# Performance work log

Hardware: AMD Instinct MI355X
Metric: run time of the kernel (lower is better)

The kernel has to match this reference:

```python
import jax, jax.numpy as jnp
import numpy as np

DIM = 256
NUM_HEADS = 4
HEAD_DIM = DIM // NUM_HEADS


def setup_inputs() -> dict:
    key = jax.random.key(0)
    ks = jax.random.split(key, 8)
    B, N, C = 4, 2048, DIM
    x = jax.random.normal(ks[0], (B, N, C), dtype=jnp.float32)
    R = jax.random.normal(ks[1], (B, 3, 3), dtype=jnp.float32)
    P = jax.random.normal(ks[2], (N, 3), dtype=jnp.float32)
    s = 1.0 / np.sqrt(C)
    qkv_w = jax.random.normal(ks[3], (3 * C, C), dtype=jnp.float32) * s
    qkv_b = jax.random.normal(ks[4], (3 * C,), dtype=jnp.float32) * 0.02
    proj_w = jax.random.normal(ks[5], (C, C), dtype=jnp.float32) * s
    proj_b = jax.random.normal(ks[6], (C,), dtype=jnp.float32) * 0.02
    pos_scale = jnp.asarray(1.0, dtype=jnp.float32)
    return {"x": x, "R": R, "P": P, "qkv_w": qkv_w, "qkv_b": qkv_b,
            "proj_w": proj_w, "proj_b": proj_b, "pos_scale": pos_scale}


def reference(x, R, P, qkv_w, qkv_b, proj_w, proj_b, pos_scale):
    B, N, C = x.shape
    H, D = NUM_HEADS, HEAD_DIM
    scale = D ** -0.5
    # qkv: (B,N,3C) -> (3,B,H,N,D)
    qkv = (x @ qkv_w.T + qkv_b).reshape(B, N, 3, H, D).transpose(2, 0, 3, 1, 4)
    q, k, v = qkv[0], qkv[1], qkv[2]
    # attention logits (B,H,N,N)
    attn = jnp.einsum('bhid,bhjd->bhij', q, k) * scale
    # positional bias: RP = (R @ P^T)^T -> (B,N,3); bias_ij = dot(RP_i, P_j)
    RP = jnp.einsum('bab,jb->bja', R, P) if False else jnp.einsum('bca,ja->bjc', jnp.swapaxes(R, 1, 2), P)
    RP = jnp.einsum('bcd,jd->bjc', R, P)  # (B,N,3): (R @ P.T).T
    bias = jnp.einsum('bik,jk->bij', RP, P)[:, None, :, :] * pos_scale  # (B,1,N,N) broadcast over heads
    attn = jax.nn.softmax(attn + bias, axis=-1)
    out = jnp.einsum('bhij,bhjd->bhid', attn, v)  # (B,H,N,D)
    out = out.transpose(0, 2, 1, 3).reshape(B, N, C)
    out = out @ proj_w.T + proj_b
    return out
```

## Files before the change

kernel.cpp:

```cpp
#include <hip/hip_runtime.h>
#include <hip/hip_bf16.h>

#define B_ 4
#define N_ 2048
#define C_ 256
#define H_ 4
#define D_ 64

typedef __attribute__((ext_vector_type(8))) short bf16x8;
typedef __attribute__((ext_vector_type(4))) float f32x4;

#define LOG2E 1.4426950408889634f

static __device__ inline unsigned short f2bf(float f) {
    unsigned u = __builtin_bit_cast(unsigned, f);
    unsigned r = (u + 0x7fffu + ((u >> 16) & 1u)) >> 16;
    return (unsigned short)r;
}
static __device__ inline float bf2f(unsigned short h) {
    unsigned u = ((unsigned)h) << 16;
    return __builtin_bit_cast(float, u);
}
static __device__ inline unsigned pack2(float a, float b) {
    __hip_bfloat162 h = __float22bfloat162_rn(make_float2(a, b));
    unsigned u;
    __builtin_memcpy(&u, &h, 4);
    return u;
}
static __device__ inline bf16x8 ld_frag(const unsigned short* p) {
    return __builtin_bit_cast(bf16x8, *(const uint4*)p);
}

__global__ __launch_bounds__(256) void prep_kernel(
    const float* __restrict__ x, const float* __restrict__ qkv_w,
    const float* __restrict__ proj_w, const float* __restrict__ Pm,
    unsigned short* __restrict__ xb, unsigned short* __restrict__ wqb,
    unsigned short* __restrict__ wpb, unsigned short* __restrict__ Pext)
{
    const int bid = blockIdx.x, tid = threadIdx.x;
    const float* s; unsigned short* d; int i;
    if (bid < 1024)      { s = x;      d = xb;  i = (bid * 256 + tid) * 8; }
    else if (bid < 1120) { s = qkv_w;  d = wqb; i = ((bid - 1024) * 256 + tid) * 8; }
    else if (bid < 1152) { s = proj_w; d = wpb; i = ((bid - 1120) * 256 + tid) * 8; }
    else {
        int n = (bid - 1152) * 256 + tid;
        if (n >= N_) return;
        unsigned short row[32];
        #pragma unroll
        for (int q = 0; q < 32; ++q) row[q] = 0;
        #pragma unroll
        for (int c = 0; c < 3; ++c) {
            float p = Pm[n * 3 + c];
            unsigned short u = f2bf(p);
            unsigned short v = f2bf(p - bf2f(u));
            row[c] = u; row[3 + c] = v; row[6 + c] = u;
        }
        #pragma unroll
        for (int q = 0; q < 4; ++q)
            *(uint4*)&Pext[(size_t)n * 32 + q * 8] = *(const uint4*)&row[q * 8];
        return;
    }
    float4 a = *(const float4*)(s + i);
    float4 b = *(const float4*)(s + i + 4);
    uint4 u;
    u.x = pack2(a.x, a.y); u.y = pack2(a.z, a.w);
    u.z = pack2(b.x, b.y); u.w = pack2(b.z, b.w);
    *(uint4*)(d + i) = u;
}

__global__ __launch_bounds__(256) void qkv_gemm(
    const unsigned short* __restrict__ xb, const unsigned short* __restrict__ wb,
    const float* __restrict__ bias, unsigned short* __restrict__ qb,
    unsigned short* __restrict__ kb, unsigned short* __restrict__ vt)
{
    __shared__ __align__(16) unsigned short As[128 * 40];
    __shared__ __align__(16) unsigned short Bs[64 * 40];
    const int m0 = blockIdx.x * 128, o0 = blockIdx.y * 64;
    const int tid = threadIdx.x;
    const int wave = tid >> 6, lane = tid & 63, quad = lane >> 4, l16 = lane & 15;

    f32x4 acc[2][4];
    #pragma unroll
    for (int i = 0; i < 2; ++i)
        #pragma unroll
        for (int j = 0; j < 4; ++j) acc[i][j] = (f32x4){0.f, 0.f, 0.f, 0.f};

    for (int k0 = 0; k0 < 256; k0 += 32) {
        __syncthreads();
        {
            int row = tid >> 1, cb = (tid & 1) * 16;
            const unsigned short* src = &xb[(size_t)(m0 + row) * 256 + k0 + cb];
            *(uint4*)&As[row * 40 + cb + 0] = *(const uint4*)(src + 0);
            *(uint4*)&As[row * 40 + cb + 8] = *(const uint4*)(src + 8);
        }
        {
            int row = tid >> 2, cb = (tid & 3) * 8;
            *(uint4*)&Bs[row * 40 + cb] = *(const uint4*)&wb[(size_t)(o0 + row) * 256 + k0 + cb];
        }
        __syncthreads();
        bf16x8 a[2], b[4];
        #pragma unroll
        for (int mt = 0; mt < 2; ++mt) a[mt] = ld_frag(&As[(wave * 32 + mt * 16 + l16) * 40 + quad * 8]);
        #pragma unroll
        for (int nt = 0; nt < 4; ++nt) b[nt] = ld_frag(&Bs[(nt * 16 + l16) * 40 + quad * 8]);
        #pragma unroll
        for (int mt = 0; mt < 2; ++mt)
            #pragma unroll
            for (int nt = 0; nt < 4; ++nt)
                acc[mt][nt] = __builtin_amdgcn_mfma_f32_16x16x32_bf16(a[mt], b[nt], acc[mt][nt], 0, 0, 0);
    }

    const int three = o0 >> 8;
    const int h = (o0 >> 6) & 3;
    const int b = m0 >> 11;
    float bv[4];
    #pragma unroll
    for (int nt = 0; nt < 4; ++nt) bv[nt] = bias[o0 + nt * 16 + l16];

    if (three == 2) {
        const int n64 = ((m0 + (wave >> 1) * 64) & 2047);
        const size_t bh64 = ((size_t)b * H_ + h) * 64;
        #pragma unroll
        for (int nt = 0; nt < 4; ++nt) {
            int d = nt * 16 + l16;
            #pragma unroll
            for (int r = 0; r < 4; ++r) {
                unsigned pw = pack2(acc[0][nt][r] + bv[nt], acc[1][nt][r] + bv[nt]);
                *(unsigned*)&vt[(bh64 + d) * N_ + n64 + 16 * quad + 4 * r + 2 * (wave & 1)] = pw;
            }
        }
    } else {
        unsigned short* dst = (three == 0) ? qb : kb;
        float sc = (three == 0) ? (0.125f * LOG2E) : 1.0f;
        #pragma unroll
        for (int mt = 0; mt < 2; ++mt)
            #pragma unroll
            for (int r = 0; r < 4; ++r) {
                int m = m0 + wave * 32 + mt * 16 + quad * 4 + r;
                int n = m & 2047;
                size_t rowbase = (((size_t)b * H_ + h) * N_ + n) * D_;
                #pragma unroll
                for (int nt = 0; nt < 4; ++nt)
                    dst[rowbase + nt * 16 + l16] = f2bf((acc[mt][nt][r] + bv[nt]) * sc);
            }
    }
}

#define LDK 72
#define LDKX 104

__global__ __launch_bounds__(256) void attn_kernel(
    const unsigned short* __restrict__ qb, const unsigned short* __restrict__ kb,
    const unsigned short* __restrict__ vt, const unsigned short* __restrict__ Pext,
    const float* __restrict__ Rm, const float* __restrict__ Pm,
    const float* __restrict__ ps_ptr,
    unsigned short* __restrict__ Opart, float* __restrict__ ml)
{
    __shared__ __align__(16) unsigned short Ks[64 * LDKX];
    __shared__ __align__(16) unsigned short Vs[64 * LDK];
    __shared__ __align__(16) unsigned short Ps[64 * LDK];

    const int bh = blockIdx.y;
    const int b = bh >> 2;
    const int i0 = blockIdx.x * 64;
    const int split = blockIdx.z;
    const int tid = threadIdx.x;
    const int wave = tid >> 6, lane = tid & 63;
    const int quad = lane >> 4, l16 = lane & 15;
    const float ps = ps_ptr[0];

    const size_t base = (size_t)bh * N_ * D_;
    const unsigned short* qg = qb + base;
    const unsigned short* kg = kb + base;
    const unsigned short* vg = vt + base;

    const int qrow = i0 + wave * 16 + l16;
    bf16x8 aq[3];
    #pragma unroll
    for (int ks = 0; ks < 2; ++ks)
        aq[ks] = ld_frag(&qg[(size_t)qrow * D_ + ks * 32 + quad * 8]);

    {
        float p0 = Pm[qrow * 3 + 0], p1 = Pm[qrow * 3 + 1], p2 = Pm[qrow * 3 + 2];
        float sc = ps * LOG2E;
        unsigned short ah[3], al[3];
        #pragma unroll
        for (int c = 0; c < 3; ++c) {
            float a = (Rm[b * 9 + c * 3 + 0] * p0 + Rm[b * 9 + c * 3 + 1] * p1
                     + Rm[b * 9 + c * 3 + 2] * p2) * sc;
            ah[c] = f2bf(a);
            al[c] = f2bf(a - bf2f(ah[c]));
        }
        bf16x8 e = (bf16x8){0,0,0,0,0,0,0,0};
        if (quad == 0) {
            e[0] = (short)ah[0]; e[1] = (short)ah[1]; e[2] = (short)ah[2];
            e[3] = (short)ah[0]; e[4] = (short)ah[1]; e[5] = (short)ah[2];
            e[6] = (short)al[0]; e[7] = (short)al[1];
        } else if (quad == 1) {
            e[0] = (short)al[2];
        }
        aq[2] = e;
    }

    const bf16x8 ones = (bf16x8){0x3F80,0x3F80,0x3F80,0x3F80,0x3F80,0x3F80,0x3F80,0x3F80};

    float m_run = -1e30f;
    f32x4 o_acc[4], lacc;
    #pragma unroll
    for (int t = 0; t < 4; ++t) o_acc[t] = (f32x4){0.f, 0.f, 0.f, 0.f};
    lacc = (f32x4){0.f, 0.f, 0.f, 0.f};

    const int jbeg = split * (N_ / 2);
    for (int jt = 0; jt < (N_ / 2) / 64; ++jt) {
        const int j0 = jbeg + jt * 64;
        __syncthreads();
        #pragma unroll
        for (int rr = 0; rr < 2; ++rr) {
            int c = tid + rr * 256;
            int row = c >> 3, off = (c & 7) * 8;
            *(uint4*)&Ks[row * LDKX + off] = *(const uint4*)&kg[(size_t)(j0 + row) * D_ + off];
            *(uint4*)&Vs[row * LDK + off] = *(const uint4*)&vg[(size_t)row * N_ + j0 + off];
        }
        {
            int row = tid >> 2, q4 = tid & 3;
            *(uint4*)&Ks[row * LDKX + 64 + q4 * 8] = *(const uint4*)&Pext[(size_t)(j0 + row) * 32 + q4 * 8];
        }
        __syncthreads();

        f32x4 s[4];
        #pragma unroll
        for (int t = 0; t < 4; ++t) {
            f32x4 c = {0.f, 0.f, 0.f, 0.f};
            #pragma unroll
            for (int ks = 0; ks < 3; ++ks) {
                bf16x8 bk = ld_frag(&Ks[(l16 + 16 * t) * LDKX + ks * 32 + quad * 8]);
                c = __builtin_amdgcn_mfma_f32_16x16x32_bf16(aq[ks], bk, c, 0, 0, 0);
            }
            s[t] = c;
        }

        float mx = m_run;
        #pragma unroll
        for (int t = 0; t < 4; ++t)
            #pragma unroll
            for (int r = 0; r < 4; ++r)
                mx = fmaxf(mx, s[t][r]);
        #pragma unroll
        for (int off = 1; off < 64; off <<= 1)
            mx = fmaxf(mx, __shfl_xor(mx, off));
        const float alpha = exp2f(m_run - mx);
        m_run = mx;

        #pragma unroll
        for (int r = 0; r < 4; ++r) {
            float p0 = exp2f(s[0][r] - mx), p1 = exp2f(s[1][r] - mx);
            float p2 = exp2f(s[2][r] - mx), p3 = exp2f(s[3][r] - mx);
            uint2 w;
            w.x = pack2(p0, p1);
            w.y = pack2(p2, p3);
            *(uint2*)&Ps[(wave * 16 + quad * 4 + r) * LDK + 4 * l16] = w;
        }

        #pragma unroll
        for (int t = 0; t < 4; ++t)
            #pragma unroll
            for (int r = 0; r < 4; ++r)
                o_acc[t][r] *= alpha;
        #pragma unroll
        for (int r = 0; r < 4; ++r) lacc[r] *= alpha;

        #pragma unroll
        for (int ks = 0; ks < 2; ++ks) {
            bf16x8 ap = ld_frag(&Ps[(wave * 16 + l16) * LDK + ks * 32 + quad * 8]);
            #pragma unroll
            for (int t = 0; t < 4; ++t) {
                bf16x8 bv = ld_frag(&Vs[(l16 + 16 * t) * LDK + ks * 32 + quad * 8]);
                o_acc[t] = __builtin_amdgcn_mfma_f32_16x16x32_bf16(ap, bv, o_acc[t], 0, 0, 0);
            }
            lacc = __builtin_amdgcn_mfma_f32_16x16x32_bf16(ap, ones, lacc, 0, 0, 0);
        }
    }

    const size_t pbase = (size_t)(split * 16 + bh) * N_;
    #pragma unroll
    for (int r = 0; r < 4; ++r) {
        int row = i0 + wave * 16 + quad * 4 + r;
        #pragma unroll
        for (int t = 0; t < 4; ++t)
            Opart[(pbase + row) * D_ + l16 + 16 * t] = f2bf(o_acc[t][r]);
        if (l16 == 0) {
            float2* mlp = (float2*)ml;
            mlp[pbase + row] = make_float2(m_run, lacc[r]);
        }
    }
}

__global__ __launch_bounds__(256) void proj_gemm(
    const unsigned short* __restrict__ Opart, const float* __restrict__ ml,
    const unsigned short* __restrict__ wb, const float* __restrict__ bias,
    float* __restrict__ out)
{
    __shared__ __align__(16) unsigned short As[64 * 40];
    __shared__ __align__(16) unsigned short Bs[64 * 40];
    const int m0 = blockIdx.x * 64, o0 = blockIdx.y * 64;
    const int tid = threadIdx.x;
    const int wave = tid >> 6, lane = tid & 63, quad = lane >> 4, l16 = lane & 15;
    const float2* mlp = (const float2*)ml;

    f32x4 acc[4];
    #pragma unroll
    for (int j = 0; j < 4; ++j) acc[j] = (f32x4){0.f, 0.f, 0.f, 0.f};

    for (int k0 = 0; k0 < 256; k0 += 32) {
        __syncthreads();
        {
            int row = tid >> 2, cb = (tid & 3) * 8;
            int m = m0 + row;
            int b = m >> 11, n = m & 2047;
            int h = k0 >> 6, d0 = (k0 & 63) + cb;
            size_t r1 = (size_t)(b * 4 + h) * N_ + n;
            size_t r2 = (size_t)(16 + b * 4 + h) * N_ + n;
            float2 ml1 = mlp[r1], ml2 = mlp[r2];
            float mm = fmaxf(ml1.x, ml2.x);
            float w1 = exp2f(ml1.x - mm), w2 = exp2f(ml2.x - mm);
            float inv = 1.f / (ml1.y * w1 + ml2.y * w2);
            w1 *= inv; w2 *= inv;
            union { uint4 u; unsigned short s[8]; } a1, a2;
            a1.u = *(const uint4*)&Opart[r1 * D_ + d0];
            a2.u = *(const uint4*)&Opart[r2 * D_ + d0];
            uint4 mv;
            unsigned* mp = (unsigned*)&mv;
            #pragma unroll
            for (int j = 0; j < 4; ++j)
                mp[j] = pack2(bf2f(a1.s[2*j]) * w1 + bf2f(a2.s[2*j]) * w2,
                              bf2f(a1.s[2*j+1]) * w1 + bf2f(a2.s[2*j+1]) * w2);
            *(uint4*)&As[row * 40 + cb] = mv;
        }
        {
            int row = tid >> 2, cb = (tid & 3) * 8;
            *(uint4*)&Bs[row * 40 + cb] = *(const uint4*)&wb[(size_t)(o0 + row) * 256 + k0 + cb];
        }
        __syncthreads();
        bf16x8 a = ld_frag(&As[(wave * 16 + l16) * 40 + quad * 8]);
        #pragma unroll
        for (int nt = 0; nt < 4; ++nt) {
            bf16x8 b = ld_frag(&Bs[(nt * 16 + l16) * 40 + quad * 8]);
            acc[nt] = __builtin_amdgcn_mfma_f32_16x16x32_bf16(a, b, acc[nt], 0, 0, 0);
        }
    }

    float bv[4];
    #pragma unroll
    for (int nt = 0; nt < 4; ++nt) bv[nt] = bias[o0 + nt * 16 + l16];
    #pragma unroll
    for (int r = 0; r < 4; ++r) {
        int m = m0 + wave * 16 + quad * 4 + r;
        #pragma unroll
        for (int nt = 0; nt < 4; ++nt)
            out[(size_t)m * 256 + o0 + nt * 16 + l16] = acc[nt][r] + bv[nt];
    }
}

extern "C" void kernel_launch(void* const* d_in, const int* in_sizes, int n_in,
                              void* d_out, int out_size, void* d_ws, size_t ws_size,
                              hipStream_t stream) {
    const float* x       = (const float*)d_in[0];
    const float* Rm      = (const float*)d_in[1];
    const float* Pm      = (const float*)d_in[2];
    const float* qkv_w   = (const float*)d_in[3];
    const float* qkv_b   = (const float*)d_in[4];
    const float* proj_w  = (const float*)d_in[5];
    const float* proj_b  = (const float*)d_in[6];
    const float* pos_scl = (const float*)d_in[7];
    float* out = (float*)d_out;

    const size_t NE = (size_t)B_ * H_ * N_ * D_;
    unsigned short* xb    = (unsigned short*)d_ws;
    unsigned short* wqb   = xb   + NE;
    unsigned short* wpb   = wqb  + 768 * 256;
    unsigned short* pext  = wpb  + 256 * 256;
    unsigned short* qb    = pext + 2048 * 32;
    unsigned short* kb    = qb   + NE;
    unsigned short* vtb   = kb   + NE;
    unsigned short* opart = vtb  + NE;
    float*          mlb   = (float*)(opart + 2 * NE);

    prep_kernel<<<1160, 256, 0, stream>>>(x, qkv_w, proj_w, Pm, xb, wqb, wpb, pext);
    qkv_gemm<<<dim3(64, 12), 256, 0, stream>>>(xb, wqb, qkv_b, qb, kb, vtb);
    attn_kernel<<<dim3(32, 16, 2), 256, 0, stream>>>(qb, kb, vtb, pext, Rm, Pm, pos_scl, opart, mlb);
    proj_gemm<<<dim3(128, 4), 256, 0, stream>>>(opart, mlb, wpb, proj_b, out);
}
```

Measured before the change: 147.8 us.

## Split attention KV into four chunks, drop LDS staging in GEMMs and V

Result: slower. 194.0 us (+31.2%).

```diff
diff --git a/kernel.cpp b/kernel.cpp
--- a/kernel.cpp
+++ b/kernel.cpp
@@ -22,10 +22,7 @@
     return __builtin_bit_cast(float, u);
 }
 static __device__ inline unsigned pack2(float a, float b) {
-    __hip_bfloat162 h = __float22bfloat162_rn(make_float2(a, b));
-    unsigned u;
-    __builtin_memcpy(&u, &h, 4);
-    return u;
+    return (unsigned)f2bf(a) | ((unsigned)f2bf(b) << 16);
 }
 static __device__ inline bf16x8 ld_frag(const unsigned short* p) {
     return __builtin_bit_cast(bf16x8, *(const uint4*)p);
@@ -73,8 +70,6 @@
     const float* __restrict__ bias, unsigned short* __restrict__ qb,
     unsigned short* __restrict__ kb, unsigned short* __restrict__ vt)
 {
-    __shared__ __align__(16) unsigned short As[128 * 40];
-    __shared__ __align__(16) unsigned short Bs[64 * 40];
     const int m0 = blockIdx.x * 128, o0 = blockIdx.y * 64;
     const int tid = threadIdx.x;
     const int wave = tid >> 6, lane = tid & 63, quad = lane >> 4, l16 = lane & 15;
@@ -85,24 +80,16 @@
         #pragma unroll
         for (int j = 0; j < 4; ++j) acc[i][j] = (f32x4){0.f, 0.f, 0.f, 0.f};
 
+    const unsigned short* arow0 = &xb[(size_t)(m0 + wave * 32 + l16) * 256 + quad * 8];
+    const unsigned short* brow0 = &wb[(size_t)(o0 + l16) * 256 + quad * 8];
+
+    #pragma unroll
     for (int k0 = 0; k0 < 256; k0 += 32) {
-        __syncthreads();
-        {
-            int row = tid >> 1, cb = (tid & 1) * 16;
-            const unsigned short* src = &xb[(size_t)(m0 + row) * 256 + k0 + cb];
-            *(uint4*)&As[row * 40 + cb + 0] = *(const uint4*)(src + 0);
-            *(uint4*)&As[row * 40 + cb + 8] = *(const uint4*)(src + 8);
-        }
-        {
-            int row = tid >> 2, cb = (tid & 3) * 8;
-            *(uint4*)&Bs[row * 40 + cb] = *(const uint4*)&wb[(size_t)(o0 + row) * 256 + k0 + cb];
-        }
-        __syncthreads();
         bf16x8 a[2], b[4];
         #pragma unroll
-        for (int mt = 0; mt < 2; ++mt) a[mt] = ld_frag(&As[(wave * 32 + mt * 16 + l16) * 40 + quad * 8]);
-        #pragma unroll
-        for (int nt = 0; nt < 4; ++nt) b[nt] = ld_frag(&Bs[(nt * 16 + l16) * 40 + quad * 8]);
+        for (int mt = 0; mt < 2; ++mt) a[mt] = ld_frag(arow0 + (size_t)mt * 16 * 256 + k0);
+        #pragma unroll
+        for (int nt = 0; nt < 4; ++nt) b[nt] = ld_frag(brow0 + (size_t)nt * 16 * 256 + k0);
         #pragma unroll
         for (int mt = 0; mt < 2; ++mt)
             #pragma unroll
@@ -157,7 +144,6 @@
     unsigned short* __restrict__ Opart, float* __restrict__ ml)
 {
     __shared__ __align__(16) unsigned short Ks[64 * LDKX];
-    __shared__ __align__(16) unsigned short Vs[64 * LDK];
     __shared__ __align__(16) unsigned short Ps[64 * LDK];
 
     const int bh = blockIdx.y;
@@ -210,8 +196,8 @@
     for (int t = 0; t < 4; ++t) o_acc[t] = (f32x4){0.f, 0.f, 0.f, 0.f};
     lacc = (f32x4){0.f, 0.f, 0.f, 0.f};
 
-    const int jbeg = split * (N_ / 2);
-    for (int jt = 0; jt < (N_ / 2) / 64; ++jt) {
+    const int jbeg = split * (N_ / 4);
+    for (int jt = 0; jt < (N_ / 4) / 64; ++jt) {
         const int j0 = jbeg + jt * 64;
         __syncthreads();
         #pragma unroll
@@ -219,7 +205,6 @@
             int c = tid + rr * 256;
             int row = c >> 3, off = (c & 7) * 8;
             *(uint4*)&Ks[row * LDKX + off] = *(const uint4*)&kg[(size_t)(j0 + row) * D_ + off];
-            *(uint4*)&Vs[row * LDK + off] = *(const uint4*)&vg[(size_t)row * N_ + j0 + off];
         }
         {
             int row = tid >> 2, q4 = tid & 3;
@@ -261,20 +246,22 @@
             *(uint2*)&Ps[(wave * 16 + quad * 4 + r) * LDK + 4 * l16] = w;
         }
 
-        #pragma unroll
-        for (int t = 0; t < 4; ++t)
-            #pragma unroll
-            for (int r = 0; r < 4; ++r)
-                o_acc[t][r] *= alpha;
-        #pragma unroll
-        for (int r = 0; r < 4; ++r) lacc[r] *= alpha;
+        if (alpha < 1.0f) {
+            #pragma unroll
+            for (int t = 0; t < 4; ++t)
+                #pragma unroll
+                for (int r = 0; r < 4; ++r)
+                    o_acc[t][r] *= alpha;
+            #pragma unroll
+            for (int r = 0; r < 4; ++r) lacc[r] *= alpha;
+        }
 
         #pragma unroll
         for (int ks = 0; ks < 2; ++ks) {
             bf16x8 ap = ld_frag(&Ps[(wave * 16 + l16) * LDK + ks * 32 + quad * 8]);
             #pragma unroll
             for (int t = 0; t < 4; ++t) {
-                bf16x8 bv = ld_frag(&Vs[(l16 + 16 * t) * LDK + ks * 32 + quad * 8]);
+                bf16x8 bv = ld_frag(&vg[(size_t)(l16 + 16 * t) * N_ + j0 + ks * 32 + quad * 8]);
                 o_acc[t] = __builtin_amdgcn_mfma_f32_16x16x32_bf16(ap, bv, o_acc[t], 0, 0, 0);
             }
             lacc = __builtin_amdgcn_mfma_f32_16x16x32_bf16(ap, ones, lacc, 0, 0, 0);
@@ -300,52 +287,54 @@
     const unsigned short* __restrict__ wb, const float* __restrict__ bias,
     float* __restrict__ out)
 {
-    __shared__ __align__(16) unsigned short As[64 * 40];
-    __shared__ __align__(16) unsigned short Bs[64 * 40];
     const int m0 = blockIdx.x * 64, o0 = blockIdx.y * 64;
     const int tid = threadIdx.x;
     const int wave = tid >> 6, lane = tid & 63, quad = lane >> 4, l16 = lane & 15;
     const float2* mlp = (const float2*)ml;
 
+    const int m = m0 + wave * 16 + l16;
+    const int b = m >> 11, n = m & 2047;
+
     f32x4 acc[4];
     #pragma unroll
     for (int j = 0; j < 4; ++j) acc[j] = (f32x4){0.f, 0.f, 0.f, 0.f};
 
-    for (int k0 = 0; k0 < 256; k0 += 32) {
-        __syncthreads();
-        {
-            int row = tid >> 2, cb = (tid & 3) * 8;
-            int m = m0 + row;
-            int b = m >> 11, n = m & 2047;
-            int h = k0 >> 6, d0 = (k0 & 63) + cb;
-            size_t r1 = (size_t)(b * 4 + h) * N_ + n;
-            size_t r2 = (size_t)(16 + b * 4 + h) * N_ + n;
-            float2 ml1 = mlp[r1], ml2 = mlp[r2];
-            float mm = fmaxf(ml1.x, ml2.x);
-            float w1 = exp2f(ml1.x - mm), w2 = exp2f(ml2.x - mm);
-            float inv = 1.f / (ml1.y * w1 + ml2.y * w2);
-            w1 *= inv; w2 *= inv;
-            union { uint4 u; unsigned short s[8]; } a1, a2;
-            a1.u = *(const uint4*)&Opart[r1 * D_ + d0];
-            a2.u = *(const uint4*)&Opart[r2 * D_ + d0];
-            uint4 mv;
-            unsigned* mp = (unsigned*)&mv;
-            #pragma unroll
-            for (int j = 0; j < 4; ++j)
-                mp[j] = pack2(bf2f(a1.s[2*j]) * w1 + bf2f(a2.s[2*j]) * w2,
-                              bf2f(a1.s[2*j+1]) * w1 + bf2f(a2.s[2*j+1]) * w2);
-            *(uint4*)&As[row * 40 + cb] = mv;
-        }
-        {
-            int row = tid >> 2, cb = (tid & 3) * 8;
-            *(uint4*)&Bs[row * 40 + cb] = *(const uint4*)&wb[(size_t)(o0 + row) * 256 + k0 + cb];
-        }
-        __syncthreads();
-        bf16x8 a = ld_frag(&As[(wave * 16 + l16) * 40 + quad * 8]);
-        #pragma unroll
-        for (int nt = 0; nt < 4; ++nt) {
-            bf16x8 b = ld_frag(&Bs[(nt * 16 + l16) * 40 + quad * 8]);
-            acc[nt] = __builtin_amdgcn_mfma_f32_16x16x32_bf16(a, b, acc[nt], 0, 0, 0);
+    #pragma unroll
+    for (int k0 = 0; k0 < 256; k0 += 64) {
+        const int h = k0 >> 6;
+        size_t rbase = (size_t)(b * 4 + h) * N_ + n;
+        float2 ml0 = mlp[rbase], ml1 = mlp[rbase + 16 * N_];
+        float2 ml2 = mlp[rbase + 32 * N_], ml3 = mlp[rbase + 48 * N_];
+        float mm = fmaxf(fmaxf(ml0.x, ml1.x), fmaxf(ml2.x, ml3.x));
+        float w0 = exp2f(ml0.x - mm), w1 = exp2f(ml1.x - mm);
+        float w2 = exp2f(ml2.x - mm), w3 = exp2f(ml3.x - mm);
+        float inv = 1.f / (ml0.y * w0 + ml1.y * w1 + ml2.y * w2 + ml3.y * w3);
+        w0 *= inv; w1 *= inv; w2 *= inv; w3 *= inv;
+
+        #pragma unroll
+        for (int kk = 0; kk < 2; ++kk) {
+            const int d0 = kk * 32 + quad * 8;
+            union { uint4 u; unsigned short s[8]; } a0, a1, a2, a3;
+            a0.u = *(const uint4*)&Opart[rbase * D_ + d0];
+            a1.u = *(const uint4*)&Opart[(rbase + 16 * N_) * D_ + d0];
+            a2.u = *(const uint4*)&Opart[(rbase + 32 * N_) * D_ + d0];
+            a3.u = *(const uint4*)&Opart[(rbase + 48 * N_) * D_ + d0];
+            uint4 av;
+            unsigned* ap = (unsigned*)&av;
+            #pragma unroll
+            for (int j = 0; j < 4; ++j) {
+                float lo = bf2f(a0.s[2*j]) * w0 + bf2f(a1.s[2*j]) * w1
+                         + bf2f(a2.s[2*j]) * w2 + bf2f(a3.s[2*j]) * w3;
+                float hi = bf2f(a0.s[2*j+1]) * w0 + bf2f(a1.s[2*j+1]) * w1
+                         + bf2f(a2.s[2*j+1]) * w2 + bf2f(a3.s[2*j+1]) * w3;
+                ap[j] = pack2(lo, hi);
+            }
+            bf16x8 a = __builtin_bit_cast(bf16x8, av);
+            #pragma unroll
+            for (int nt = 0; nt < 4; ++nt) {
+                bf16x8 bfrag = ld_frag(&wb[(size_t)(o0 + nt * 16 + l16) * 256 + k0 + kk * 32 + quad * 8]);
+                acc[nt] = __builtin_amdgcn_mfma_f32_16x16x32_bf16(a, bfrag, acc[nt], 0, 0, 0);
+            }
         }
     }
 
@@ -354,10 +343,10 @@
     for (int nt = 0; nt < 4; ++nt) bv[nt] = bias[o0 + nt * 16 + l16];
     #pragma unroll
     for (int r = 0; r < 4; ++r) {
-        int m = m0 + wave * 16 + quad * 4 + r;
+        int mo = m0 + wave * 16 + quad * 4 + r;
         #pragma unroll
         for (int nt = 0; nt < 4; ++nt)
-            out[(size_t)m * 256 + o0 + nt * 16 + l16] = acc[nt][r] + bv[nt];
+            out[(size_t)mo * 256 + o0 + nt * 16 + l16] = acc[nt][r] + bv[nt];
     }
 }
 
@@ -383,10 +372,10 @@
     unsigned short* kb    = qb   + NE;
     unsigned short* vtb   = kb   + NE;
     unsigned short* opart = vtb  + NE;
-    float*          mlb   = (float*)(opart + 2 * NE);
+    float*          mlb   = (float*)(opart + 4 * NE);
 
     prep_kernel<<<1160, 256, 0, stream>>>(x, qkv_w, proj_w, Pm, xb, wqb, wpb, pext);
     qkv_gemm<<<dim3(64, 12), 256, 0, stream>>>(xb, wqb, qkv_b, qb, kb, vtb);
-    attn_kernel<<<dim3(32, 16, 2), 256, 0, stream>>>(qb, kb, vtb, pext, Rm, Pm, pos_scl, opart, mlb);
+    attn_kernel<<<dim3(32, 16, 4), 256, 0, stream>>>(qb, kb, vtb, pext, Rm, Pm, pos_scl, opart, mlb);
     proj_gemm<<<dim3(128, 4), 256, 0, stream>>>(opart, mlb, wpb, proj_b, out);
 }
```

## Enlarge QKV GEMM tile, compute P extension in attention, hoist merge weights

Applied to the files above, without the earlier changes.

New measurement: 140.1 us. 1.06x faster.

```diff
diff --git a/kernel.cpp b/kernel.cpp
--- a/kernel.cpp
+++ b/kernel.cpp
@@ -31,35 +31,17 @@
     return __builtin_bit_cast(bf16x8, *(const uint4*)p);
 }
 
-__global__ __launch_bounds__(256) void prep_kernel(
+__global__ __launch_bounds__(256) void cvt_kernel(
     const float* __restrict__ x, const float* __restrict__ qkv_w,
-    const float* __restrict__ proj_w, const float* __restrict__ Pm,
+    const float* __restrict__ proj_w,
     unsigned short* __restrict__ xb, unsigned short* __restrict__ wqb,
-    unsigned short* __restrict__ wpb, unsigned short* __restrict__ Pext)
+    unsigned short* __restrict__ wpb)
 {
     const int bid = blockIdx.x, tid = threadIdx.x;
     const float* s; unsigned short* d; int i;
     if (bid < 1024)      { s = x;      d = xb;  i = (bid * 256 + tid) * 8; }
     else if (bid < 1120) { s = qkv_w;  d = wqb; i = ((bid - 1024) * 256 + tid) * 8; }
-    else if (bid < 1152) { s = proj_w; d = wpb; i = ((bid - 1120) * 256 + tid) * 8; }
-    else {
-        int n = (bid - 1152) * 256 + tid;
-        if (n >= N_) return;
-        unsigned short row[32];
-        #pragma unroll
-        for (int q = 0; q < 32; ++q) row[q] = 0;
-        #pragma unroll
-        for (int c = 0; c < 3; ++c) {
-            float p = Pm[n * 3 + c];
-            unsigned short u = f2bf(p);
-            unsigned short v = f2bf(p - bf2f(u));
-            row[c] = u; row[3 + c] = v; row[6 + c] = u;
-        }
-        #pragma unroll
-        for (int q = 0; q < 4; ++q)
-            *(uint4*)&Pext[(size_t)n * 32 + q * 8] = *(const uint4*)&row[q * 8];
-        return;
-    }
+    else                 { s = proj_w; d = wpb; i = ((bid - 1120) * 256 + tid) * 8; }
     float4 a = *(const float4*)(s + i);
     float4 b = *(const float4*)(s + i + 4);
     uint4 u;
@@ -74,70 +56,75 @@
     unsigned short* __restrict__ kb, unsigned short* __restrict__ vt)
 {
     __shared__ __align__(16) unsigned short As[128 * 40];
-    __shared__ __align__(16) unsigned short Bs[64 * 40];
-    const int m0 = blockIdx.x * 128, o0 = blockIdx.y * 64;
+    __shared__ __align__(16) unsigned short Bs[128 * 40];
+    const int m0 = blockIdx.x * 128, o0 = blockIdx.y * 128;
     const int tid = threadIdx.x;
     const int wave = tid >> 6, lane = tid & 63, quad = lane >> 4, l16 = lane & 15;
-
-    f32x4 acc[2][4];
-    #pragma unroll
-    for (int i = 0; i < 2; ++i)
+    const int wy = wave >> 1, wx = wave & 1;
+
+    f32x4 acc[4][4];
+    #pragma unroll
+    for (int i = 0; i < 4; ++i)
         #pragma unroll
         for (int j = 0; j < 4; ++j) acc[i][j] = (f32x4){0.f, 0.f, 0.f, 0.f};
 
+    const int srow = tid >> 1, soff = (tid & 1) * 16;
+
     for (int k0 = 0; k0 < 256; k0 += 32) {
         __syncthreads();
         {
-            int row = tid >> 1, cb = (tid & 1) * 16;
-            const unsigned short* src = &xb[(size_t)(m0 + row) * 256 + k0 + cb];
-            *(uint4*)&As[row * 40 + cb + 0] = *(const uint4*)(src + 0);
-            *(uint4*)&As[row * 40 + cb + 8] = *(const uint4*)(src + 8);
-        }
-        {
-            int row = tid >> 2, cb = (tid & 3) * 8;
-            *(uint4*)&Bs[row * 40 + cb] = *(const uint4*)&wb[(size_t)(o0 + row) * 256 + k0 + cb];
-        }
-        __syncthreads();
-        bf16x8 a[2], b[4];
-        #pragma unroll
-        for (int mt = 0; mt < 2; ++mt) a[mt] = ld_frag(&As[(wave * 32 + mt * 16 + l16) * 40 + quad * 8]);
-        #pragma unroll
-        for (int nt = 0; nt < 4; ++nt) b[nt] = ld_frag(&Bs[(nt * 16 + l16) * 40 + quad * 8]);
-        #pragma unroll
-        for (int mt = 0; mt < 2; ++mt)
+            const unsigned short* sa = &xb[(size_t)(m0 + srow) * 256 + k0 + soff];
+            const unsigned short* sb = &wb[(size_t)(o0 + srow) * 256 + k0 + soff];
+            *(uint4*)&As[srow * 40 + soff + 0] = *(const uint4*)(sa + 0);
+            *(uint4*)&As[srow * 40 + soff + 8] = *(const uint4*)(sa + 8);
+            *(uint4*)&Bs[srow * 40 + soff + 0] = *(const uint4*)(sb + 0);
+            *(uint4*)&Bs[srow * 40 + soff + 8] = *(const uint4*)(sb + 8);
+        }
+        __syncthreads();
+        bf16x8 a[4], b[4];
+        #pragma unroll
+        for (int mt = 0; mt < 4; ++mt) a[mt] = ld_frag(&As[(wy * 64 + mt * 16 + l16) * 40 + quad * 8]);
+        #pragma unroll
+        for (int nt = 0; nt < 4; ++nt) b[nt] = ld_frag(&Bs[(wx * 64 + nt * 16 + l16) * 40 + quad * 8]);
+        #pragma unroll
+        for (int mt = 0; mt < 4; ++mt)
             #pragma unroll
             for (int nt = 0; nt < 4; ++nt)
                 acc[mt][nt] = __builtin_amdgcn_mfma_f32_16x16x32_bf16(a[mt], b[nt], acc[mt][nt], 0, 0, 0);
     }
 
-    const int three = o0 >> 8;
-    const int h = (o0 >> 6) & 3;
+    const int sec = o0 + wx * 64;
+    const int three = sec >> 8;
+    const int h = (sec >> 6) & 3;
     const int b = m0 >> 11;
     float bv[4];
     #pragma unroll
-    for (int nt = 0; nt < 4; ++nt) bv[nt] = bias[o0 + nt * 16 + l16];
+    for (int nt = 0; nt < 4; ++nt) bv[nt] = bias[sec + nt * 16 + l16];
 
     if (three == 2) {
-        const int n64 = ((m0 + (wave >> 1) * 64) & 2047);
+        const int n64 = (m0 + wy * 64) & 2047;
         const size_t bh64 = ((size_t)b * H_ + h) * 64;
         #pragma unroll
         for (int nt = 0; nt < 4; ++nt) {
             int d = nt * 16 + l16;
             #pragma unroll
             for (int r = 0; r < 4; ++r) {
-                unsigned pw = pack2(acc[0][nt][r] + bv[nt], acc[1][nt][r] + bv[nt]);
-                *(unsigned*)&vt[(bh64 + d) * N_ + n64 + 16 * quad + 4 * r + 2 * (wave & 1)] = pw;
+                ushort4 v;
+                v.x = f2bf(acc[0][nt][r] + bv[nt]);
+                v.y = f2bf(acc[1][nt][r] + bv[nt]);
+                v.z = f2bf(acc[2][nt][r] + bv[nt]);
+                v.w = f2bf(acc[3][nt][r] + bv[nt]);
+                *(ushort4*)&vt[(bh64 + d) * N_ + n64 + 16 * quad + 4 * r] = v;
             }
         }
     } else {
         unsigned short* dst = (three == 0) ? qb : kb;
         float sc = (three == 0) ? (0.125f * LOG2E) : 1.0f;
         #pragma unroll
-        for (int mt = 0; mt < 2; ++mt)
+        for (int mt = 0; mt < 4; ++mt)
             #pragma unroll
             for (int r = 0; r < 4; ++r) {
-                int m = m0 + wave * 32 + mt * 16 + quad * 4 + r;
-                int n = m & 2047;
+                int n = (m0 + wy * 64 + mt * 16 + quad * 4 + r) & 2047;
                 size_t rowbase = (((size_t)b * H_ + h) * N_ + n) * D_;
                 #pragma unroll
                 for (int nt = 0; nt < 4; ++nt)
@@ -151,7 +138,7 @@
 
 __global__ __launch_bounds__(256) void attn_kernel(
     const unsigned short* __restrict__ qb, const unsigned short* __restrict__ kb,
-    const unsigned short* __restrict__ vt, const unsigned short* __restrict__ Pext,
+    const unsigned short* __restrict__ vt,
     const float* __restrict__ Rm, const float* __restrict__ Pm,
     const float* __restrict__ ps_ptr,
     unsigned short* __restrict__ Opart, float* __restrict__ ml)
@@ -174,6 +161,12 @@
     const unsigned short* kg = kb + base;
     const unsigned short* vg = vt + base;
 
+    if (tid < 64) {
+        uint4 z = {0u, 0u, 0u, 0u};
+        *(uint4*)&Ks[tid * LDKX + 80] = z;
+        *(uint4*)&Ks[tid * LDKX + 88] = z;
+    }
+
     const int qrow = i0 + wave * 16 + l16;
     bf16x8 aq[3];
     #pragma unroll
@@ -211,7 +204,9 @@
     lacc = (f32x4){0.f, 0.f, 0.f, 0.f};
 
     const int jbeg = split * (N_ / 2);
-    for (int jt = 0; jt < (N_ / 2) / 64; ++jt) {
+    const int NT = (N_ / 2) / 64;
+
+    for (int jt = 0; jt < NT; ++jt) {
         const int j0 = jbeg + jt * 64;
         __syncthreads();
         #pragma unroll
@@ -221,9 +216,19 @@
             *(uint4*)&Ks[row * LDKX + off] = *(const uint4*)&kg[(size_t)(j0 + row) * D_ + off];
             *(uint4*)&Vs[row * LDK + off] = *(const uint4*)&vg[(size_t)row * N_ + j0 + off];
         }
-        {
-            int row = tid >> 2, q4 = tid & 3;
-            *(uint4*)&Ks[row * LDKX + 64 + q4 * 8] = *(const uint4*)&Pext[(size_t)(j0 + row) * 32 + q4 * 8];
+        if (tid < 64) {
+            const float* pp = &Pm[(size_t)(j0 + tid) * 3];
+            float p0 = pp[0], p1 = pp[1], p2 = pp[2];
+            unsigned u0 = f2bf(p0), u1 = f2bf(p1), u2 = f2bf(p2);
+            unsigned v0 = f2bf(p0 - bf2f((unsigned short)u0));
+            unsigned v1 = f2bf(p1 - bf2f((unsigned short)u1));
+            unsigned v2 = f2bf(p2 - bf2f((unsigned short)u2));
+            uint4 lo, hi;
+            lo.x = u0 | (u1 << 16); lo.y = u2 | (v0 << 16);
+            lo.z = v1 | (v2 << 16); lo.w = u0 | (u1 << 16);
+            hi.x = u2; hi.y = 0u; hi.z = 0u; hi.w = 0u;
+            *(uint4*)&Ks[tid * LDKX + 64] = lo;
+            *(uint4*)&Ks[tid * LDKX + 72] = hi;
         }
         __syncthreads();
 
@@ -261,13 +266,15 @@
             *(uint2*)&Ps[(wave * 16 + quad * 4 + r) * LDK + 4 * l16] = w;
         }
 
-        #pragma unroll
-        for (int t = 0; t < 4; ++t)
-            #pragma unroll
-            for (int r = 0; r < 4; ++r)
-                o_acc[t][r] *= alpha;
-        #pragma unroll
-        for (int r = 0; r < 4; ++r) lacc[r] *= alpha;
+        if (alpha < 1.0f) {
+            #pragma unroll
+            for (int t = 0; t < 4; ++t)
+                #pragma unroll
+                for (int r = 0; r < 4; ++r)
+                    o_acc[t][r] *= alpha;
+            #pragma unroll
+            for (int r = 0; r < 4; ++r) lacc[r] *= alpha;
+        }
 
         #pragma unroll
         for (int ks = 0; ks < 2; ++ks) {
@@ -307,38 +314,42 @@
     const int wave = tid >> 6, lane = tid & 63, quad = lane >> 4, l16 = lane & 15;
     const float2* mlp = (const float2*)ml;
 
+    const int srow = tid >> 2, scb = (tid & 3) * 8;
+    const int sm = m0 + srow, sb = sm >> 11, sn = sm & 2047;
+
+    float w1h[4], w2h[4];
+    #pragma unroll
+    for (int h = 0; h < 4; ++h) {
+        size_t r1 = (size_t)(sb * 4 + h) * N_ + sn;
+        float2 ml1 = mlp[r1], ml2 = mlp[r1 + 16 * N_];
+        float mm = fmaxf(ml1.x, ml2.x);
+        float w1 = exp2f(ml1.x - mm), w2 = exp2f(ml2.x - mm);
+        float inv = 1.f / (ml1.y * w1 + ml2.y * w2);
+        w1h[h] = w1 * inv; w2h[h] = w2 * inv;
+    }
+
     f32x4 acc[4];
     #pragma unroll
     for (int j = 0; j < 4; ++j) acc[j] = (f32x4){0.f, 0.f, 0.f, 0.f};
 
     for (int k0 = 0; k0 < 256; k0 += 32) {
+        const int h = k0 >> 6;
+        const int d0 = (k0 & 63) + scb;
         __syncthreads();
         {
-            int row = tid >> 2, cb = (tid & 3) * 8;
-            int m = m0 + row;
-            int b = m >> 11, n = m & 2047;
-            int h = k0 >> 6, d0 = (k0 & 63) + cb;
-            size_t r1 = (size_t)(b * 4 + h) * N_ + n;
-            size_t r2 = (size_t)(16 + b * 4 + h) * N_ + n;
-            float2 ml1 = mlp[r1], ml2 = mlp[r2];
-            float mm = fmaxf(ml1.x, ml2.x);
-            float w1 = exp2f(ml1.x - mm), w2 = exp2f(ml2.x - mm);
-            float inv = 1.f / (ml1.y * w1 + ml2.y * w2);
-            w1 *= inv; w2 *= inv;
+            size_t r1 = (size_t)(sb * 4 + h) * N_ + sn;
             union { uint4 u; unsigned short s[8]; } a1, a2;
             a1.u = *(const uint4*)&Opart[r1 * D_ + d0];
-            a2.u = *(const uint4*)&Opart[r2 * D_ + d0];
+            a2.u = *(const uint4*)&Opart[(r1 + 16 * N_) * D_ + d0];
+            float w1 = w1h[h], w2 = w2h[h];
             uint4 mv;
             unsigned* mp = (unsigned*)&mv;
             #pragma unroll
             for (int j = 0; j < 4; ++j)
                 mp[j] = pack2(bf2f(a1.s[2*j]) * w1 + bf2f(a2.s[2*j]) * w2,
                               bf2f(a1.s[2*j+1]) * w1 + bf2f(a2.s[2*j+1]) * w2);
-            *(uint4*)&As[row * 40 + cb] = mv;
-        }
-        {
-            int row = tid >> 2, cb = (tid & 3) * 8;
-            *(uint4*)&Bs[row * 40 + cb] = *(const uint4*)&wb[(size_t)(o0 + row) * 256 + k0 + cb];
+            *(uint4*)&As[srow * 40 + scb] = mv;
+            *(uint4*)&Bs[srow * 40 + scb] = *(const uint4*)&wb[(size_t)(o0 + srow) * 256 + k0 + scb];
         }
         __syncthreads();
         bf16x8 a = ld_frag(&As[(wave * 16 + l16) * 40 + quad * 8]);
@@ -378,15 +389,14 @@
     unsigned short* xb    = (unsigned short*)d_ws;
     unsigned short* wqb   = xb   + NE;
     unsigned short* wpb   = wqb  + 768 * 256;
-    unsigned short* pext  = wpb  + 256 * 256;
-    unsigned short* qb    = pext + 2048 * 32;
+    unsigned short* qb    = wpb  + 256 * 256;
     unsigned short* kb    = qb   + NE;
     unsigned short* vtb   = kb   + NE;
     unsigned short* opart = vtb  + NE;
     float*          mlb   = (float*)(opart + 2 * NE);
 
-    prep_kernel<<<1160, 256, 0, stream>>>(x, qkv_w, proj_w, Pm, xb, wqb, wpb, pext);
-    qkv_gemm<<<dim3(64, 12), 256, 0, stream>>>(xb, wqb, qkv_b, qb, kb, vtb);
-    attn_kernel<<<dim3(32, 16, 2), 256, 0, stream>>>(qb, kb, vtb, pext, Rm, Pm, pos_scl, opart, mlb);
+    cvt_kernel<<<1152, 256, 0, stream>>>(x, qkv_w, proj_w, xb, wqb, wpb);
+    qkv_gemm<<<dim3(64, 6), 256, 0, stream>>>(xb, wqb, qkv_b, qb, kb, vtb);
+    attn_kernel<<<dim3(32, 16, 2), 256, 0, stream>>>(qb, kb, vtb, Rm, Pm, pos_scl, opart, mlb);
     proj_gemm<<<dim3(128, 4), 256, 0, stream>>>(opart, mlb, wpb, proj_b, out);
 }
```
